# Kernel tuning notes

Hardware: AMD Instinct MI355X
Metric: run time of the kernel (lower is better)

Reference implementation:

```python
import jax, jax.numpy as jnp
import numpy as np

LEAK = 0.01  # F.leaky_relu default negative_slope
TAU = 1.0    # sinkhorn_tau
ITERS = 5    # sinkhorn_iters


def leaky_relu(x):
    return jnp.where(x >= 0, x, LEAK * x)


def setup_inputs() -> dict:
    key = jax.random.key(0)
    B, N, F, E, H, L = 512, 200, 32, 128, 128, 2
    ks = jax.random.split(key, 8)
    def s(k, shape, fan_in):
        return jax.random.normal(k, shape, dtype=jnp.float32) * (1.0 / np.sqrt(fan_in)).astype(np.float32)
    return {
        "x": jax.random.normal(ks[0], (B, N, F), dtype=jnp.float32),
        "w_emb": s(ks[1], (E, F), F),
        "b_emb": jnp.zeros((E,), jnp.float32),
        "w_ih": s(ks[2], (L, 4 * H, E), H),   # stacked per-layer LSTM input weights
        "w_hh": s(ks[3], (L, 4 * H, H), H),   # stacked per-layer LSTM recurrent weights
        "b_ih": jnp.zeros((L, 4 * H), jnp.float32),
        "b_hh": jnp.zeros((L, 4 * H), jnp.float32),
        "w_fc1": s(ks[4], (E, H), H),
        "b_fc1": jnp.zeros((E,), jnp.float32),
        "w_fc2": s(ks[5], (N, E), E),
        "b_fc2": jnp.zeros((N,), jnp.float32),
        "do_round": 0,  # non-differentiable Hungarian rounding path disabled
    }


def _lstm_layer(xs, h0, c0, Wih, Whh, b):
    # xs: [N, B, E]  (seq-major, like torch.nn.LSTM); h0, c0: [B, H]
    def step(carry, x_t):
        h, c = carry
        g = x_t @ Wih.T + h @ Whh.T + b               # [B, 4H]
        i, f, gg, o = jnp.split(g, 4, axis=-1)        # torch gate order i,f,g,o
        c = jax.nn.sigmoid(f) * c + jax.nn.sigmoid(i) * jnp.tanh(gg)
        h = jax.nn.sigmoid(o) * jnp.tanh(c)
        return (h, c), h
    (hN, cN), hs = jax.lax.scan(step, (h0, c0), xs)
    return hs, hN, cN


def _sinkhorn(M, tau, n_iters):
    # exp(M / tau) followed by alternating row / column normalization
    x = jnp.exp(M / tau)
    for _ in range(n_iters):
        x = x / jnp.sum(x, axis=2, keepdims=True)  # row normalize
        x = x / jnp.sum(x, axis=1, keepdims=True)  # column normalize
    return x


def reference(x, w_emb, b_emb, w_ih, w_hh, b_ih, b_hh, w_fc1, b_fc1, w_fc2, b_fc2, do_round):
    # do_round=0: the Hungarian rounding branch (host round-trip) is skipped;
    # the module then returns just the Sinkhorn output psi.
    B = x.shape[0]
    H = w_hh.shape[-1]
    e = leaky_relu(x @ w_emb.T + b_emb)            # [B, N, E]
    xs = jnp.transpose(e, (1, 0, 2))               # [N, B, E]
    h = jnp.zeros((B, H), x.dtype)
    c = jnp.zeros((B, H), x.dtype)
    hs = xs
    # NB: original code feeds the SAME embedded x to every LSTM layer,
    # carrying only the (h, c) state between layers.
    for l in range(w_ih.shape[0]):
        hs, h, c = _lstm_layer(xs, h, c, w_ih[l], w_hh[l], b_ih[l] + b_hh[l])
    out = jnp.transpose(hs, (1, 0, 2))             # [B, N, H]
    out = leaky_relu(out @ w_fc1.T + b_fc1)        # [B, N, E]
    M = out @ w_fc2.T + b_fc2                      # [B, N, N]
    psi = _sinkhorn(M, TAU, ITERS)
    return psi
```

## Files before the change

### kernel.cpp

```cpp
#include <hip/hip_runtime.h>
#include <cstdint>
#include <cstddef>

#define LEAK 0.01f
#define L2E 1.4426950408889634f

typedef _Float16 f16;
typedef __attribute__((ext_vector_type(4))) _Float16 f16x4;
typedef __attribute__((ext_vector_type(8))) _Float16 f16x8;
typedef __attribute__((ext_vector_type(4))) float f32x4;

static __device__ __forceinline__ f16x8 pack8s(float4 a, float4 b, float s) {
  f16x8 r;
  r[0] = (f16)(a.x * s); r[1] = (f16)(a.y * s); r[2] = (f16)(a.z * s); r[3] = (f16)(a.w * s);
  r[4] = (f16)(b.x * s); r[5] = (f16)(b.y * s); r[6] = (f16)(b.z * s); r[7] = (f16)(b.w * s);
  return r;
}
static __device__ __forceinline__ f16x8 pack8(float4 a, float4 b) {
  return pack8s(a, b, 1.0f);
}
#define MFMA16(a, b, c) __builtin_amdgcn_mfma_f32_16x16x32_f16((a), (b), (c), 0, 0, 0)

__constant__ float SCG[4] = {L2E, L2E, 2.0f * L2E, L2E};

__global__ __launch_bounds__(256) void k_emb(
    const float* __restrict__ x, const float* __restrict__ wemb,
    const float* __restrict__ bemb, f16* __restrict__ e) {
  const int t = blockIdx.x, tid = threadIdx.x;
  __shared__ __align__(16) float wl[128 * 32];
  __shared__ float bl[128];
  for (int idx = tid; idx < 1024; idx += 256)
    ((float4*)wl)[idx] = ((const float4*)wemb)[idx];
  if (tid < 128) bl[tid] = bemb[tid];

  float xa[32], xb[32];
  const float* xpa = x + ((size_t)tid * 200 + t) * 32;
  const float* xpb = x + ((size_t)(tid + 256) * 200 + t) * 32;
#pragma unroll
  for (int k4 = 0; k4 < 8; ++k4) {
    float4 va = *(const float4*)(xpa + k4 * 4);
    float4 vb = *(const float4*)(xpb + k4 * 4);
    xa[k4 * 4 + 0] = va.x; xa[k4 * 4 + 1] = va.y; xa[k4 * 4 + 2] = va.z; xa[k4 * 4 + 3] = va.w;
    xb[k4 * 4 + 0] = vb.x; xb[k4 * 4 + 1] = vb.y; xb[k4 * 4 + 2] = vb.z; xb[k4 * 4 + 3] = vb.w;
  }
  __syncthreads();

  f16* ea = e + ((size_t)t * 512 + tid) * 128;
  f16* eb = e + ((size_t)t * 512 + tid + 256) * 128;
  for (int j8 = 0; j8 < 16; ++j8) {
    f16x8 oa, ob;
#pragma unroll
    for (int jj = 0; jj < 8; ++jj) {
      int j = j8 * 8 + jj;
      float aa = bl[j], ab = bl[j];
#pragma unroll
      for (int k4 = 0; k4 < 8; ++k4) {
        float4 wv = *(const float4*)&wl[j * 32 + k4 * 4];
        aa += xa[k4 * 4 + 0] * wv.x + xa[k4 * 4 + 1] * wv.y +
              xa[k4 * 4 + 2] * wv.z + xa[k4 * 4 + 3] * wv.w;
        ab += xb[k4 * 4 + 0] * wv.x + xb[k4 * 4 + 1] * wv.y +
              xb[k4 * 4 + 2] * wv.z + xb[k4 * 4 + 3] * wv.w;
      }
      oa[jj] = (f16)(aa >= 0.f ? aa : LEAK * aa);
      ob[jj] = (f16)(ab >= 0.f ? ab : LEAK * ab);
    }
    *(f16x8*)(ea + j8 * 8) = oa;
    *(f16x8*)(eb + j8 * 8) = ob;
  }
}

static __device__ __forceinline__ void xp_waves(
    const f16* __restrict__ e, const float* __restrict__ wih,
    const float* __restrict__ bih, const float* __restrict__ bhh,
    f16* __restrict__ xp, int t0, int wid, int nrep, int stride, int lane) {
  const int q = lane >> 4, l16 = lane & 15;
  const int ct = wid & 7;

  f16x8 BW[4][4];
  float bias[4];
#pragma unroll
  for (int G = 0; G < 4; ++G) {
    int n = G * 128 + ct * 16 + l16;
    bias[G] = (bih[n] + bhh[n]) * SCG[G];
#pragma unroll
    for (int kc = 0; kc < 4; ++kc) {
      const float4* p = (const float4*)(wih + (size_t)n * 128 + kc * 32 + q * 8);
      BW[G][kc] = pack8s(p[0], p[1], SCG[G]);
    }
  }
  for (int rep = 0; rep < nrep; ++rep) {
    int task = wid + rep * stride;
    int g2 = task >> 3;
    int tl = g2 >> 2, btg = g2 & 3;
#pragma unroll
    for (int p = 0; p < 8; ++p) {
      int bt = btg * 8 + p;
      const f16* A = e + ((size_t)(t0 + tl) * 512 + bt * 16 + l16) * 128 + q * 8;
      f16x8 af[4];
#pragma unroll
      for (int kc = 0; kc < 4; ++kc) af[kc] = *(const f16x8*)(A + kc * 32);
      f32x4 acc[4];
#pragma unroll
      for (int G = 0; G < 4; ++G)
        acc[G] = (f32x4){bias[G], bias[G], bias[G], bias[G]};
#pragma unroll
      for (int kc = 0; kc < 4; ++kc)
#pragma unroll
        for (int G = 0; G < 4; ++G)
          acc[G] = MFMA16(af[kc], BW[G][kc], acc[G]);
      f16x8 oA, oB;
#pragma unroll
      for (int r = 0; r < 4; ++r) {
        oA[r]     = (f16)acc[0][r];
        oA[4 + r] = (f16)acc[1][r];
        oB[r]     = (f16)acc[2][r];
        oB[4 + r] = (f16)acc[3][r];
      }
      f16* dst = xp + (size_t)tl * 262144 + bt * 8192 + ct * 1024 + lane * 16;
      *(f16x8*)dst = oA;
      *(f16x8*)(dst + 8) = oB;
    }
  }
}

__global__ __launch_bounds__(256, 2) void k_xp(
    const f16* __restrict__ e, const float* __restrict__ wih,
    const float* __restrict__ bih, const float* __restrict__ bhh,
    f16* __restrict__ xp, int t0) {
  xp_waves(e, wih, bih, bhh, xp, t0,
           blockIdx.x * 4 + (threadIdx.x >> 6), 1, 0, threadIdx.x & 63);
}

static __device__ __forceinline__ void rec_body(
    const f16* __restrict__ xp, const float* __restrict__ whh,
    float* __restrict__ hws, float* __restrict__ cws,
    f16* __restrict__ hs, int layer, int t0, int CH, int bt) {
  const int tid = threadIdx.x;
  const int w = tid >> 6, lane = tid & 63, q = lane >> 4, l16 = lane & 15;
  __shared__ __align__(16) f16 hlds[2][16][136];

  f16x8 BH[4][4];
#pragma unroll
  for (int G = 0; G < 4; ++G) {
    int n = G * 128 + w * 16 + l16;
#pragma unroll
    for (int kc = 0; kc < 4; ++kc) {
      const float4* ph = (const float4*)(whh + (size_t)n * 128 + kc * 32 + q * 8);
      BH[G][kc] = pack8s(ph[0], ph[1], SCG[G]);
    }
  }

  f32x4 cst;
  if (layer == 0 && t0 == 0) {
    cst = (f32x4){0.f, 0.f, 0.f, 0.f};
    for (int idx = tid; idx < 2 * 16 * 136; idx += 512)
      ((f16*)hlds)[idx] = (f16)0.f;
  } else {
    cst = *(const f32x4*)(cws + ((size_t)(bt * 8 + w) * 64 + lane) * 4);
    f32x4 hv = *(const f32x4*)(hws + ((size_t)(bt * 8 + w) * 64 + lane) * 4);
#pragma unroll
    for (int r = 0; r < 4; ++r)
      hlds[1][q * 4 + r][w * 16 + l16] = (f16)hv[r];
  }
  __syncthreads();

  const f16* xpl = xp + (((size_t)bt * 8 + w) * 64 + lane) * 16;
  f16x8 xa = *(const f16x8*)(xpl);
  f16x8 xb = *(const f16x8*)(xpl + 8);

  f32x4 hk;
  const int srow = tid >> 5, scol = (tid & 31) * 4;
  for (int tl = 0; tl < CH; ++tl) {
    int tn = (tl + 1 < CH) ? tl + 1 : tl;
    const f16* xpn = xpl + (size_t)tn * 262144;
    f16x8 nxa = *(const f16x8*)(xpn);
    f16x8 nxb = *(const f16x8*)(xpn + 8);

    const int rb = (tl + 1) & 1;
    f16x8 ah[4];
#pragma unroll
    for (int kc = 0; kc < 4; ++kc)
      ah[kc] = *(const f16x8*)&hlds[rb][l16][kc * 32 + q * 8];

    f32x4 acc[4];
#pragma unroll
    for (int r = 0; r < 4; ++r) {
      acc[0][r] = (float)xa[r];
      acc[1][r] = (float)xa[4 + r];
      acc[2][r] = (float)xb[r];
      acc[3][r] = (float)xb[4 + r];
    }
#pragma unroll
    for (int kc = 0; kc < 4; ++kc)
#pragma unroll
      for (int G = 0; G < 4; ++G)
        acc[G] = MFMA16(ah[kc], BH[G][kc], acc[G]);

    const int wb = tl & 1;
#pragma unroll
    for (int r = 0; r < 4; ++r) {
      float ui = __builtin_amdgcn_exp2f(-acc[0][r]);
      float uf = __builtin_amdgcn_exp2f(-acc[1][r]);
      float ug = __builtin_amdgcn_exp2f(-fmaxf(acc[2][r], -88.f));
      float uo = __builtin_amdgcn_exp2f(-acc[3][r]);
      float sf = __builtin_amdgcn_rcpf(1.0f + uf);
      float p1 = (1.0f - ug) * __builtin_amdgcn_rcpf((1.0f + ui) * (1.0f + ug));
      float cc = sf * cst[r] + p1;
      cst[r] = cc;
      float ccl = fminf(fmaxf(cc, -30.f), 30.f) * (-2.0f * L2E);
      float ucc = __builtin_amdgcn_exp2f(ccl);
      float hv = (1.0f - ucc) * __builtin_amdgcn_rcpf((1.0f + uo) * (1.0f + ucc));
      hk[r] = hv;
      hlds[wb][q * 4 + r][w * 16 + l16] = (f16)hv;
    }
    __syncthreads();
    if (layer != 0) {
      f16x4 hv4 = *(const f16x4*)&hlds[wb][srow][scol];
      *(f16x4*)(hs + ((size_t)(bt * 16 + srow) * 200 + (t0 + tl)) * 128 + scol) = hv4;
    }
    xa = nxa; xb = nxb;
  }

  *(f32x4*)(hws + ((size_t)(bt * 8 + w) * 64 + lane) * 4) = hk;
  *(f32x4*)(cws + ((size_t)(bt * 8 + w) * 64 + lane) * 4) = cst;
}

__global__ __launch_bounds__(512, 2) void k_rec(
    const f16* __restrict__ xp, const float* __restrict__ whh,
    float* __restrict__ hws, float* __restrict__ cws,
    f16* __restrict__ hs, int layer, int t0, int CH) {
  rec_body(xp, whh, hws, cws, hs, layer, t0, CH, blockIdx.x);
}

__global__ __launch_bounds__(512, 2) void k_recxp(
    const f16* __restrict__ xp_r, const float* __restrict__ whh,
    float* __restrict__ hws, float* __restrict__ cws,
    f16* __restrict__ hs, int layer, int t0_r,
    const f16* __restrict__ e, const float* __restrict__ wih_n,
    const float* __restrict__ bih_n, const float* __restrict__ bhh_n,
    f16* __restrict__ xp_w, int t0_x) {
  if (blockIdx.x < 32) {
    rec_body(xp_r, whh, hws, cws, hs, layer, t0_r, 100, blockIdx.x);
  } else {
    xp_waves(e, wih_n, bih_n, bhh_n, xp_w, t0_x,
             (blockIdx.x - 32) * 8 + (threadIdx.x >> 6), 2, 1600,
             threadIdx.x & 63);
  }
}

__global__ __launch_bounds__(512, 4) void k_head(
    const f16* __restrict__ hs, const float* __restrict__ wfc1,
    const float* __restrict__ bfc1, const float* __restrict__ wfc2,
    const float* __restrict__ bfc2, float* __restrict__ psi) {
  extern __shared__ char smem[];
  f16* E = (f16*)smem;
  f16* o1 = (f16*)(smem + 27200);
  float* uu = (float*)(smem + 80000);
  float* vv = (float*)(smem + 80800);
  const int b = blockIdx.x, tid = threadIdx.x;
  const int w = tid >> 6, lane = tid & 63, q = lane >> 4, l16 = lane & 15;
  const f16* A = hs + (size_t)b * 200 * 128;

  f16x8 BF1[4];
  float bias1;
  {
    int n = w * 16 + l16;
    bias1 = bfc1[n];
#pragma unroll
    for (int kc = 0; kc < 4; ++kc) {
      const float4* p = (const float4*)(wfc1 + (size_t)n * 128 + kc * 32 + q * 8);
      BF1[kc] = pack8(p[0], p[1]);
    }
  }
  f16x8 BF2[2][4];
  float bias2[2] = {0.f, 0.f};
#pragma unroll
  for (int ci = 0; ci < 2; ++ci) {
    int ct = w + ci * 8;
    if (ct < 13) {
      int n = ct * 16 + l16; if (n > 199) n = 199;
      bias2[ci] = bfc2[n];
#pragma unroll
      for (int kc = 0; kc < 4; ++kc) {
        const float4* p = (const float4*)(wfc2 + (size_t)n * 128 + kc * 32 + q * 8);
        BF2[ci][kc] = pack8(p[0], p[1]);
      }
    }
  }

  for (int rt = 0; rt < 13; ++rt) {
    int m = rt * 16 + l16; if (m > 199) m = 199;
    f16x8 af[4];
#pragma unroll
    for (int kc = 0; kc < 4; ++kc)
      af[kc] = *(const f16x8*)(A + (size_t)m * 128 + kc * 32 + q * 8);
    f32x4 acc = (f32x4){bias1, bias1, bias1, bias1};
#pragma unroll
    for (int kc = 0; kc < 4; ++kc) acc = MFMA16(af[kc], BF1[kc], acc);
    int col = w * 16 + l16;
#pragma unroll
    for (int r = 0; r < 4; ++r) {
      int row = rt * 16 + q * 4 + r;
      float vvv = acc[r]; vvv = vvv >= 0.f ? vvv : LEAK * vvv;
      if (row < 200) o1[row * 136 + col] = (f16)vvv;
    }
  }
  __syncthreads();

  for (int rt = 0; rt < 13; ++rt) {
    int m = rt * 16 + l16; if (m > 199) m = 199;
    f16x8 af[4];
#pragma unroll
    for (int kc = 0; kc < 4; ++kc)
      af[kc] = *(const f16x8*)&o1[m * 136 + kc * 32 + q * 8];
    __syncthreads();
#pragma unroll
    for (int ci = 0; ci < 2; ++ci) {
      int ct = w + ci * 8;
      if (ct < 13) {
        f32x4 acc = (f32x4){bias2[ci], bias2[ci], bias2[ci], bias2[ci]};
#pragma unroll
        for (int kc = 0; kc < 4; ++kc) acc = MFMA16(af[kc], BF2[ci][kc], acc);
        int col = ct * 16 + l16;
#pragma unroll
        for (int r = 0; r < 4; ++r) {
          int row = rt * 16 + q * 4 + r;
          if (row < 200 && col < 200) E[row * 200 + col] = (f16)__expf(acc[r]);
        }
      }
    }
  }
  __syncthreads();
  if (tid < 200) vv[tid] = 1.0f;
  __syncthreads();

  for (int it = 0; it < 5; ++it) {
    if (tid < 400) {
      int r = tid >> 1, h = tid & 1;
      const f16* Er = E + r * 200 + h * 100;
      const float* vp = vv + h * 100;
      float s0 = 0.f, s1 = 0.f;
      for (int j = 0; j < 100; j += 4) {
        f16x4 e4 = *(const f16x4*)(Er + j);
        float4 v4 = *(const float4*)(vp + j);
        s0 += (float)e4[0] * v4.x + (float)e4[1] * v4.y;
        s1 += (float)e4[2] * v4.z + (float)e4[3] * v4.w;
      }
      float s = s0 + s1;
      s += __shfl_xor(s, 1);
      if (h == 0) uu[r] = __builtin_amdgcn_rcpf(s);
    }
    __syncthreads();
    if (tid < 400) {
      int c4 = tid >> 3, g = tid & 7;
      const f16* Ec = E + (size_t)(g * 25) * 200 + c4 * 4;
      float a0 = 0.f, a1 = 0.f, a2 = 0.f, a3 = 0.f;
      for (int i = 0; i < 25; ++i) {
        f16x4 e4 = *(const f16x4*)(Ec + i * 200);
        float ui = uu[g * 25 + i];
        a0 += (float)e4[0] * ui;
        a1 += (float)e4[1] * ui;
        a2 += (float)e4[2] * ui;
        a3 += (float)e4[3] * ui;
      }
#pragma unroll
      for (int mk = 1; mk <= 4; mk <<= 1) {
        a0 += __shfl_xor(a0, mk);
        a1 += __shfl_xor(a1, mk);
        a2 += __shfl_xor(a2, mk);
        a3 += __shfl_xor(a3, mk);
      }
      if (g == 0) {
        float4 o;
        o.x = __builtin_amdgcn_rcpf(a0);
        o.y = __builtin_amdgcn_rcpf(a1);
        o.z = __builtin_amdgcn_rcpf(a2);
        o.w = __builtin_amdgcn_rcpf(a3);
        *(float4*)(vv + c4 * 4) = o;
      }
    }
    __syncthreads();
  }

  float* P = psi + (size_t)b * 40000;
  for (int idx4 = tid; idx4 < 10000; idx4 += 512) {
    unsigned i = ((unsigned)idx4 * 5243u) >> 18;
    unsigned jq = (unsigned)idx4 - i * 50u;
    f16x4 e4 = *(const f16x4*)(E + i * 200 + jq * 4);
    float4 v4 = *(const float4*)(vv + jq * 4);
    float ui = uu[i];
    float4 o;
    o.x = ui * (float)e4[0] * v4.x;
    o.y = ui * (float)e4[1] * v4.y;
    o.z = ui * (float)e4[2] * v4.z;
    o.w = ui * (float)e4[3] * v4.w;
    *(float4*)(P + i * 200 + jq * 4) = o;
  }
}

extern "C" void kernel_launch(void* const* d_in, const int* in_sizes, int n_in,
                              void* d_out, int out_size, void* d_ws, size_t ws_size,
                              hipStream_t stream) {
  const float* x    = (const float*)d_in[0];
  const float* wemb = (const float*)d_in[1];
  const float* bemb = (const float*)d_in[2];
  const float* wih  = (const float*)d_in[3];
  const float* whh  = (const float*)d_in[4];
  const float* bih  = (const float*)d_in[5];
  const float* bhh  = (const float*)d_in[6];
  const float* wfc1 = (const float*)d_in[7];
  const float* bfc1 = (const float*)d_in[8];
  const float* wfc2 = (const float*)d_in[9];
  const float* bfc2 = (const float*)d_in[10];
  float* psi = (float*)d_out;

  char* ws = (char*)d_ws;
  f16*   e   = (f16*)(ws);
  float* hws = (float*)(ws + 26214400);
  float* cws = (float*)(ws + 26476544);
  f16*   hs  = (f16*)(ws + 26738688);
  f16*   xpA = (f16*)(ws + 52953088);
  f16*   xpB = (f16*)(ws + 105381888);

  const size_t fixed = 52953088;
  const bool pipelined = (ws_size >= 157810688ull);

  (void)hipFuncSetAttribute((const void*)k_head,
                            hipFuncAttributeMaxDynamicSharedMemorySize, 81600);

  k_emb<<<200, 256, 0, stream>>>(x, wemb, bemb, e);

  const float* wih1 = wih + 65536;  const float* whh1 = whh + 65536;
  const float* bih1 = bih + 512;    const float* bhh1 = bhh + 512;

  if (pipelined) {
    k_xp<<<800, 256, 0, stream>>>(e, wih, bih, bhh, xpA, 0);
    k_recxp<<<232, 512, 0, stream>>>(xpA, whh, hws, cws, hs, 0, 0,
                                     e, wih, bih, bhh, xpB, 100);
    k_recxp<<<232, 512, 0, stream>>>(xpB, whh, hws, cws, hs, 0, 100,
                                     e, wih1, bih1, bhh1, xpA, 0);
    k_recxp<<<232, 512, 0, stream>>>(xpA, whh1, hws, cws, hs, 1, 0,
                                     e, wih1, bih1, bhh1, xpB, 100);
    k_rec<<<32, 512, 0, stream>>>(xpB, whh1, hws, cws, hs, 1, 100, 100);
  } else {
    const int cands[] = {100, 50, 40, 25, 20, 10, 8, 5, 4, 2, 1};
    int CH = 1;
    for (int ci = 0; ci < 11; ++ci) {
      if (fixed + (size_t)cands[ci] * 524288 <= ws_size) { CH = cands[ci]; break; }
    }
    for (int l = 0; l < 2; ++l) {
      const float* wih_l = wih + (size_t)l * 65536;
      const float* whh_l = whh + (size_t)l * 65536;
      const float* bih_l = bih + (size_t)l * 512;
      const float* bhh_l = bhh + (size_t)l * 512;
      for (int t0 = 0; t0 < 200; t0 += CH) {
        k_xp<<<CH * 8, 256, 0, stream>>>(e, wih_l, bih_l, bhh_l, xpA, t0);
        k_rec<<<32, 512, 0, stream>>>(xpA, whh_l, hws, cws, hs, l, t0, CH);
      }
    }
  }
  k_head<<<512, 512, 81600, stream>>>(hs, wfc1, bfc1, wfc2, bfc2, psi);
}
```

Measured before the change: 609.0 us.

## Split LSTM recurrence across twice as many blocks with 8 batch rows each

The recurrent kernel now handles 8 batch rows per block instead of 16, doubling the recurrence grid from 32 to 64 blocks. Half of each MFMA's A rows are zero-padded, and results from the upper rows are moved down with cross-lane shuffles so each lane does two elementwise updates instead of four. This spreads the serial time loop over more compute units and halves per-step elementwise latency, at the cost of wasting half the MFMA work and adding shuffles. The xp indexing and the h/c state layout are remapped to match.

```diff
diff --git a/kernel.cpp b/kernel.cpp
--- a/kernel.cpp
+++ b/kernel.cpp
@@ -137,7 +137,8 @@
     f16* __restrict__ hs, int layer, int t0, int CH, int bt) {
   const int tid = threadIdx.x;
   const int w = tid >> 6, lane = tid & 63, q = lane >> 4, l16 = lane & 15;
-  __shared__ __align__(16) f16 hlds[2][16][136];
+  const int row0 = (q & 1) * 4 + (q >> 1) * 2;
+  __shared__ __align__(16) f16 hlds[2][8][136];
 
   f16x8 BH[4][4];
 #pragma unroll
@@ -150,26 +151,26 @@
     }
   }
 
-  f32x4 cst;
+  float cst0, cst1;
   if (layer == 0 && t0 == 0) {
-    cst = (f32x4){0.f, 0.f, 0.f, 0.f};
-    for (int idx = tid; idx < 2 * 16 * 136; idx += 512)
-      ((f16*)hlds)[idx] = (f16)0.f;
+    cst0 = 0.f; cst1 = 0.f;
+    for (int idx = tid; idx < 8 * 136; idx += 512)
+      (&hlds[1][0][0])[idx] = (f16)0.f;
   } else {
-    cst = *(const f32x4*)(cws + ((size_t)(bt * 8 + w) * 64 + lane) * 4);
-    f32x4 hv = *(const f32x4*)(hws + ((size_t)(bt * 8 + w) * 64 + lane) * 4);
-#pragma unroll
-    for (int r = 0; r < 4; ++r)
-      hlds[1][q * 4 + r][w * 16 + l16] = (f16)hv[r];
+    const float* cp = cws + ((size_t)(bt * 8 + w) * 64 + lane) * 2;
+    cst0 = cp[0]; cst1 = cp[1];
+    const float* hp = hws + ((size_t)(bt * 8 + w) * 64 + lane) * 2;
+    hlds[1][row0 + 0][w * 16 + l16] = (f16)hp[0];
+    hlds[1][row0 + 1][w * 16 + l16] = (f16)hp[1];
   }
   __syncthreads();
 
-  const f16* xpl = xp + (((size_t)bt * 8 + w) * 64 + lane) * 16;
+  const int qo = (bt & 1) * 2 + (q & 1);
+  const f16* xpl = xp + (((size_t)(bt >> 1) * 8 + w) * 64 + qo * 16 + l16) * 16;
   f16x8 xa = *(const f16x8*)(xpl);
   f16x8 xb = *(const f16x8*)(xpl + 8);
 
-  f32x4 hk;
-  const int srow = tid >> 5, scol = (tid & 31) * 4;
+  float hk0 = 0.f, hk1 = 0.f;
   for (int tl = 0; tl < CH; ++tl) {
     int tn = (tl + 1 < CH) ? tl + 1 : tl;
     const f16* xpn = xpl + (size_t)tn * 262144;
@@ -178,9 +179,17 @@
 
     const int rb = (tl + 1) & 1;
     f16x8 ah[4];
-#pragma unroll
-    for (int kc = 0; kc < 4; ++kc)
-      ah[kc] = *(const f16x8*)&hlds[rb][l16][kc * 32 + q * 8];
+    if (l16 < 8) {
+#pragma unroll
+      for (int kc = 0; kc < 4; ++kc)
+        ah[kc] = *(const f16x8*)&hlds[rb][l16][kc * 32 + q * 8];
+    } else {
+#pragma unroll
+      for (int kc = 0; kc < 4; ++kc) {
+#pragma unroll
+        for (int i = 0; i < 8; ++i) ah[kc][i] = (f16)0.f;
+      }
+    }
 
     f32x4 acc[4];
 #pragma unroll
@@ -196,33 +205,50 @@
       for (int G = 0; G < 4; ++G)
         acc[G] = MFMA16(ah[kc], BH[G][kc], acc[G]);
 
+    float e0[4], e1[4];
+#pragma unroll
+    for (int G = 0; G < 4; ++G) {
+      float s2 = __shfl_xor(acc[G][2], 32);
+      float s3 = __shfl_xor(acc[G][3], 32);
+      e0[G] = (q < 2) ? acc[G][0] : s2;
+      e1[G] = (q < 2) ? acc[G][1] : s3;
+    }
+
     const int wb = tl & 1;
 #pragma unroll
-    for (int r = 0; r < 4; ++r) {
-      float ui = __builtin_amdgcn_exp2f(-acc[0][r]);
-      float uf = __builtin_amdgcn_exp2f(-acc[1][r]);
-      float ug = __builtin_amdgcn_exp2f(-fmaxf(acc[2][r], -88.f));
-      float uo = __builtin_amdgcn_exp2f(-acc[3][r]);
+    for (int j = 0; j < 2; ++j) {
+      float gi = j ? e1[0] : e0[0];
+      float gf = j ? e1[1] : e0[1];
+      float gg = j ? e1[2] : e0[2];
+      float go = j ? e1[3] : e0[3];
+      float cprev = j ? cst1 : cst0;
+      float ui = __builtin_amdgcn_exp2f(-gi);
+      float uf = __builtin_amdgcn_exp2f(-gf);
+      float ug = __builtin_amdgcn_exp2f(-fmaxf(gg, -88.f));
+      float uo = __builtin_amdgcn_exp2f(-go);
       float sf = __builtin_amdgcn_rcpf(1.0f + uf);
       float p1 = (1.0f - ug) * __builtin_amdgcn_rcpf((1.0f + ui) * (1.0f + ug));
-      float cc = sf * cst[r] + p1;
-      cst[r] = cc;
+      float cc = sf * cprev + p1;
+      if (j) cst1 = cc; else cst0 = cc;
       float ccl = fminf(fmaxf(cc, -30.f), 30.f) * (-2.0f * L2E);
       float ucc = __builtin_amdgcn_exp2f(ccl);
       float hv = (1.0f - ucc) * __builtin_amdgcn_rcpf((1.0f + uo) * (1.0f + ucc));
-      hk[r] = hv;
-      hlds[wb][q * 4 + r][w * 16 + l16] = (f16)hv;
+      if (j) hk1 = hv; else hk0 = hv;
+      hlds[wb][row0 + j][w * 16 + l16] = (f16)hv;
     }
     __syncthreads();
-    if (layer != 0) {
+    if (layer != 0 && tid < 256) {
+      const int srow = tid >> 5, scol = (tid & 31) * 4;
       f16x4 hv4 = *(const f16x4*)&hlds[wb][srow][scol];
-      *(f16x4*)(hs + ((size_t)(bt * 16 + srow) * 200 + (t0 + tl)) * 128 + scol) = hv4;
+      *(f16x4*)(hs + ((size_t)(bt * 8 + srow) * 200 + (t0 + tl)) * 128 + scol) = hv4;
     }
     xa = nxa; xb = nxb;
   }
 
-  *(f32x4*)(hws + ((size_t)(bt * 8 + w) * 64 + lane) * 4) = hk;
-  *(f32x4*)(cws + ((size_t)(bt * 8 + w) * 64 + lane) * 4) = cst;
+  float* hp = hws + ((size_t)(bt * 8 + w) * 64 + lane) * 2;
+  hp[0] = hk0; hp[1] = hk1;
+  float* cp = cws + ((size_t)(bt * 8 + w) * 64 + lane) * 2;
+  cp[0] = cst0; cp[1] = cst1;
 }
 
 __global__ __launch_bounds__(512, 2) void k_rec(
@@ -239,11 +265,11 @@
     const f16* __restrict__ e, const float* __restrict__ wih_n,
     const float* __restrict__ bih_n, const float* __restrict__ bhh_n,
     f16* __restrict__ xp_w, int t0_x) {
-  if (blockIdx.x < 32) {
+  if (blockIdx.x < 64) {
     rec_body(xp_r, whh, hws, cws, hs, layer, t0_r, 100, blockIdx.x);
   } else {
     xp_waves(e, wih_n, bih_n, bhh_n, xp_w, t0_x,
-             (blockIdx.x - 32) * 8 + (threadIdx.x >> 6), 2, 1600,
+             (blockIdx.x - 64) * 8 + (threadIdx.x >> 6), 2, 1600,
              threadIdx.x & 63);
   }
 }
@@ -435,13 +461,13 @@
 
   if (pipelined) {
     k_xp<<<800, 256, 0, stream>>>(e, wih, bih, bhh, xpA, 0);
-    k_recxp<<<232, 512, 0, stream>>>(xpA, whh, hws, cws, hs, 0, 0,
+    k_recxp<<<264, 512, 0, stream>>>(xpA, whh, hws, cws, hs, 0, 0,
                                      e, wih, bih, bhh, xpB, 100);
-    k_recxp<<<232, 512, 0, stream>>>(xpB, whh, hws, cws, hs, 0, 100,
+    k_recxp<<<264, 512, 0, stream>>>(xpB, whh, hws, cws, hs, 0, 100,
                                      e, wih1, bih1, bhh1, xpA, 0);
-    k_recxp<<<232, 512, 0, stream>>>(xpA, whh1, hws, cws, hs, 1, 0,
+    k_recxp<<<264, 512, 0, stream>>>(xpA, whh1, hws, cws, hs, 1, 0,
                                      e, wih1, bih1, bhh1, xpB, 100);
-    k_rec<<<32, 512, 0, stream>>>(xpB, whh1, hws, cws, hs, 1, 100, 100);
+    k_rec<<<64, 512, 0, stream>>>(xpB, whh1, hws, cws, hs, 1, 100, 100);
   } else {
     const int cands[] = {100, 50, 40, 25, 20, 10, 8, 5, 4, 2, 1};
     int CH = 1;
@@ -455,7 +481,7 @@
       const float* bhh_l = bhh + (size_t)l * 512;
       for (int t0 = 0; t0 < 200; t0 += CH) {
         k_xp<<<CH * 8, 256, 0, stream>>>(e, wih_l, bih_l, bhh_l, xpA, t0);
-        k_rec<<<32, 512, 0, stream>>>(xpA, whh_l, hws, cws, hs, l, t0, CH);
+        k_rec<<<64, 512, 0, stream>>>(xpA, whh_l, hws, cws, hs, l, t0, CH);
       }
     }
   }
```

New measurement: 572.0 us. -6.1%, faster.
